# Kernel optimization log

Hardware: AMD Instinct MI355X
Metric: run time of the kernel (lower is better)

Reference implementation:

```python
import jax, jax.numpy as jnp
import numpy as np

QLEN, BSZ, D_MODEL = 1024, 4, 1024
N_HEAD, D_HEAD = 16, 64
RLEN = QLEN  # rlen == klen -> classic _rel_shift path
LN_EPS = 1e-5


def setup_inputs() -> dict:
    key = jax.random.key(0)
    ks = jax.random.split(key, 9)
    s = 0.02
    w = jax.random.normal(ks[0], (QLEN, BSZ, D_MODEL), jnp.float32)
    r = jax.random.normal(ks[1], (RLEN, D_MODEL), jnp.float32)
    # causal mask: True = masked (future positions)
    attn_mask = jnp.triu(jnp.ones((QLEN, QLEN), jnp.bool_), k=1)
    qkv_w = jax.random.normal(ks[2], (D_MODEL, 3 * N_HEAD * D_HEAD), jnp.float32) * s
    r_w = jax.random.normal(ks[3], (D_MODEL, N_HEAD * D_HEAD), jnp.float32) * s
    o_w = jax.random.normal(ks[4], (N_HEAD * D_HEAD, D_MODEL), jnp.float32) * s
    r_r_bias = jax.random.normal(ks[5], (N_HEAD, D_HEAD), jnp.float32) * s
    r_w_bias = jax.random.normal(ks[6], (N_HEAD, D_HEAD), jnp.float32) * s
    ln_g = jnp.ones((D_MODEL,), jnp.float32)
    ln_b = jnp.zeros((D_MODEL,), jnp.float32)
    return {"w": w, "r": r, "attn_mask": attn_mask, "qkv_w": qkv_w,
            "r_w": r_w, "o_w": o_w, "r_r_bias": r_r_bias,
            "r_w_bias": r_w_bias, "ln_g": ln_g, "ln_b": ln_b}


def _rel_shift(x):
    # x: [qlen, klen, bsz, n_head] -> Transformer-XL relative shift
    q, k, b, n = x.shape
    zero_pad = jnp.zeros((q, 1, b, n), x.dtype)
    x_padded = jnp.concatenate([zero_pad, x], axis=1)      # [q, k+1, b, n]
    x_padded = x_padded.reshape(k + 1, q, b, n)
    return x_padded[1:].reshape(q, k, b, n)


def _layer_norm(x, g, b):
    mu = jnp.mean(x, axis=-1, keepdims=True)
    var = jnp.mean(jnp.square(x - mu), axis=-1, keepdims=True)
    return (x - mu) * jax.lax.rsqrt(var + LN_EPS) * g + b


def reference(w, r, attn_mask, qkv_w, r_w, o_w, r_r_bias, r_w_bias, ln_g, ln_b):
    qlen, bsz, _ = w.shape
    H, D = r_r_bias.shape
    scale = 1.0 / D ** 0.5

    w_heads = w @ qkv_w                                    # [q, b, 3*H*D]
    q_h, k_h, v_h = jnp.split(w_heads, 3, axis=-1)
    q_h = q_h.reshape(qlen, bsz, H, D)
    k_h = k_h.reshape(qlen, bsz, H, D)
    v_h = v_h.reshape(qlen, bsz, H, D)
    r_k = (r @ r_w).reshape(-1, H, D)                      # [rlen, H, D]

    AC = jnp.einsum('ibnd,jbnd->ijbn', q_h + r_w_bias, k_h)
    BD = _rel_shift(jnp.einsum('ibnd,jnd->ijbn', q_h + r_r_bias, r_k))
    score = (AC + BD) * scale                              # [q, k, b, n]
    score = jnp.where(attn_mask[:, :, None, None], -1e30, score)

    prob = jax.nn.softmax(score, axis=1)
    vec = jnp.einsum('ijbn,jbnd->ibnd', prob, v_h).reshape(qlen, bsz, H * D)
    attn_out = vec @ o_w
    return _layer_norm(w + attn_out, ln_g, ln_b)
```

## Files before the change

kernel.cpp:

```cpp
#include <hip/hip_runtime.h>
#include <hip/hip_bf16.h>

#define SEQ    1024
#define BSZW   4
#define DMODEL 1024
#define NHEAD  16
#define DHEAD  64
#define MROWS  (SEQ*BSZW)
#define QKVN   (3*NHEAD*DHEAD)

typedef __attribute__((ext_vector_type(8))) short short8;
typedef __attribute__((ext_vector_type(4))) float f32x4;

__device__ __forceinline__ float bf2f(short s) {
    union { int i; float f; } u; u.i = ((int)(unsigned short)s) << 16; return u.f;
}
__device__ __forceinline__ short f2bf(float f) {
    union { float f; unsigned int u; } v; v.f = f;
    unsigned int r = v.u + 0x7FFFu + ((v.u >> 16) & 1u);
    return (short)(unsigned short)(r >> 16);
}

__device__ __forceinline__ void async16(const void* g, void* s) {
    __builtin_amdgcn_global_load_lds(
        (__attribute__((address_space(1))) void*)(g),
        (__attribute__((address_space(3))) void*)(s), 16, 0, 0);
}

__global__ __launch_bounds__(256) void conv_all(const float* __restrict__ w,
                                                const float* __restrict__ r,
                                                short* __restrict__ Wb,
                                                short* __restrict__ rb)
{
    int bx = blockIdx.x;
    const float* in; short* out; int idx;
    if (bx < 4096) { in = w; out = Wb; idx = (bx * 256 + threadIdx.x) * 4; }
    else           { in = r; out = rb; idx = ((bx - 4096) * 256 + threadIdx.x) * 4; }
    float4 v = *(const float4*)(in + idx);
    out[idx + 0] = f2bf(v.x);
    out[idx + 1] = f2bf(v.y);
    out[idx + 2] = f2bf(v.z);
    out[idx + 3] = f2bf(v.w);
}

__global__ __launch_bounds__(256) void trans_all(const float* __restrict__ qkv_w,
                                                 const float* __restrict__ r_w,
                                                 const float* __restrict__ o_w,
                                                 short* __restrict__ QKVt,
                                                 short* __restrict__ RWt,
                                                 short* __restrict__ OWt)
{
    const int z = blockIdx.z;
    const int bx = blockIdx.x, by = blockIdx.y;
    const float* in; short* out; int C;
    if (z == 0)      { in = qkv_w; out = QKVt; C = QKVN; }
    else if (z == 1) { in = r_w;   out = RWt;  C = DMODEL; if (bx >= 32) return; }
    else             { in = o_w;   out = OWt;  C = DMODEL; if (bx >= 32) return; }
    const int R = DMODEL;
    __shared__ short t[32][33];
    const int tid = threadIdx.x;
    const int r = tid >> 5, c = tid & 31;
    #pragma unroll
    for (int rr = 0; rr < 4; ++rr) {
        int rl = r + rr * 8;
        t[c][rl] = f2bf(in[(size_t)(by * 32 + rl) * C + bx * 32 + c]);
    }
    __syncthreads();
    #pragma unroll
    for (int rr = 0; rr < 4; ++rr) {
        int rl = r + rr * 8;
        out[(size_t)(bx * 32 + rl) * R + by * 32 + c] = t[rl][c];
    }
}

__global__ __launch_bounds__(256) void vtrans(const short* __restrict__ in,
                                              short* __restrict__ out)
{
    __shared__ short t[32][33];
    const int tid = threadIdx.x;
    const int r = tid >> 5, c = tid & 31;
    const int bx = blockIdx.x, by = blockIdx.y, bh = blockIdx.z;
    #pragma unroll
    for (int rr = 0; rr < 4; ++rr) {
        int rl = r + rr * 8;
        t[c][rl] = in[((size_t)bh * SEQ + bx * 32 + rl) * DHEAD + by * 32 + c];
    }
    __syncthreads();
    #pragma unroll
    for (int rr = 0; rr < 4; ++rr) {
        int rl = r + rr * 8;
        out[((size_t)bh * DHEAD + by * 32 + rl) * SEQ + bx * 32 + c] = t[rl][c];
    }
}

#define GEMM_LDS_CORE(A_, Bt_, K_)                                              \
    __shared__ short As[128 * 32];                                              \
    __shared__ short Bs[128 * 32];                                              \
    const int tid = threadIdx.x;                                                \
    const int w = tid >> 6, lane = tid & 63;                                    \
    const int L15 = lane & 15, quad = lane >> 4;                                \
    const int n0 = blockIdx.x * 128, m0 = blockIdx.y * 128;                     \
    const int mq = (w & 1) * 64, nq = (w >> 1) * 64;                            \
    f32x4 acc[4][4];                                                            \
    _Pragma("unroll")                                                           \
    for (int i = 0; i < 4; ++i)                                                 \
        _Pragma("unroll")                                                       \
        for (int j = 0; j < 4; ++j) acc[i][j] = (f32x4){0.f, 0.f, 0.f, 0.f};    \
    const int srow  = w * 16 + (lane >> 2);          \
    const int schnk = ((lane & 3) ^ (lane >> 4)) * 8;  \
    const int rpA = (quad ^ (L15 >> 2)) * 8;         \
    for (int k0 = 0; k0 < K_; k0 += 32) {                                       \
        __syncthreads();                                                        \
        _Pragma("unroll")                                                       \
        for (int q = 0; q < 2; ++q) {                                           \
            async16(A_ + (size_t)(m0 + q * 64 + srow) * K_ + k0 + schnk,        \
                    &As[(q * 64 + w * 16) * 32]);                               \
            async16(Bt_ + (size_t)(n0 + q * 64 + srow) * K_ + k0 + schnk,       \
                    &Bs[(q * 64 + w * 16) * 32]);                               \
        }                                                                       \
        __syncthreads();                                                        \
        short8 a[4], b[4];                                                      \
        _Pragma("unroll")                                                       \
        for (int rt = 0; rt < 4; ++rt)                                          \
            a[rt] = *(const short8*)&As[(mq + rt * 16 + L15) * 32 + rpA];       \
        _Pragma("unroll")                                                       \
        for (int ct = 0; ct < 4; ++ct)                                          \
            b[ct] = *(const short8*)&Bs[(nq + ct * 16 + L15) * 32 + rpA];       \
        _Pragma("unroll")                                                       \
        for (int rt = 0; rt < 4; ++rt)                                          \
            _Pragma("unroll")                                                   \
            for (int ct = 0; ct < 4; ++ct)                                      \
                acc[rt][ct] = __builtin_amdgcn_mfma_f32_16x16x32_bf16(          \
                    a[rt], b[ct], acc[rt][ct], 0, 0, 0);                        \
    }

__global__ __launch_bounds__(256) void qkv_mfma(const short* __restrict__ A,
                                                const short* __restrict__ Bt,
                                                const float* __restrict__ rwb,
                                                const float* __restrict__ rrb,
                                                short* __restrict__ Qwb,
                                                short* __restrict__ Qrb,
                                                short* __restrict__ Kb,
                                                short* __restrict__ Vb)
{
    GEMM_LDS_CORE(A, Bt, 1024)
    const int nb = n0 + nq;
    const int chunk = nb >> 10;
    const int h = (nb >> 6) & 15;
    float rw4[4], rr4[4];
    if (chunk == 0) {
        #pragma unroll
        for (int ct = 0; ct < 4; ++ct) {
            rw4[ct] = rwb[h * DHEAD + ct * 16 + L15];
            rr4[ct] = rrb[h * DHEAD + ct * 16 + L15];
        }
    }
    #pragma unroll
    for (int rt = 0; rt < 4; ++rt)
        #pragma unroll
        for (int g = 0; g < 4; ++g) {
            int m = m0 + mq + rt * 16 + quad * 4 + g;
            int qi = m >> 2, b = m & 3;
            size_t rowbase = ((size_t)(b * NHEAD + h) * SEQ + qi) * DHEAD;
            #pragma unroll
            for (int ct = 0; ct < 4; ++ct) {
                int d = ct * 16 + L15;
                float v = acc[rt][ct][g];
                if (chunk == 0) {
                    Qwb[rowbase + d] = f2bf(v + rw4[ct]);
                    Qrb[rowbase + d] = f2bf(v + rr4[ct]);
                } else if (chunk == 1) {
                    Kb[rowbase + d] = f2bf(v);
                } else {
                    Vb[rowbase + d] = f2bf(v);
                }
            }
        }
}

__global__ __launch_bounds__(256) void rk_mfma(const short* __restrict__ A,
                                               const short* __restrict__ Bt,
                                               short* __restrict__ RK)
{
    GEMM_LDS_CORE(A, Bt, 1024)
    const int h = (n0 + nq) >> 6;
    #pragma unroll
    for (int rt = 0; rt < 4; ++rt)
        #pragma unroll
        for (int g = 0; g < 4; ++g) {
            int m = m0 + mq + rt * 16 + quad * 4 + g;
            #pragma unroll
            for (int ct = 0; ct < 4; ++ct) {
                int d = ct * 16 + L15;
                RK[((size_t)h * SEQ + m) * DHEAD + d] = f2bf(acc[rt][ct][g]);
            }
        }
}

__global__ __launch_bounds__(256) void oproj_mfma(const short* __restrict__ A,
                                                  const short* __restrict__ Bt,
                                                  float* __restrict__ C)
{
    GEMM_LDS_CORE(A, Bt, 1024)
    #pragma unroll
    for (int rt = 0; rt < 4; ++rt)
        #pragma unroll
        for (int g = 0; g < 4; ++g) {
            int m = m0 + mq + rt * 16 + quad * 4 + g;
            #pragma unroll
            for (int ct = 0; ct < 4; ++ct)
                C[(size_t)m * DMODEL + n0 + nq + ct * 16 + L15] = acc[rt][ct][g];
        }
}

__global__ __launch_bounds__(256) void attn_mfma(const short* __restrict__ Qw,
                                                 const short* __restrict__ Qr,
                                                 const short* __restrict__ Kg,
                                                 const short* __restrict__ Vt,
                                                 const short* __restrict__ RK,
                                                 short* __restrict__ ATT)
{
    __shared__ short Ks[2][64 * 64];
    __shared__ short Vts[2][64 * 64];
    __shared__ short Pbuf[4][16][136];

    const int tid  = threadIdx.x;
    const int w    = tid >> 6;
    const int lane = tid & 63;
    const int L15  = lane & 15;
    const int quad = lane >> 4;
    const int bh   = blockIdx.x;
    const int itA  = blockIdx.y;
    const int itB  = 15 - itA;
    const int h    = bh & (NHEAD - 1);
    const int b    = bh >> 4;
    const int C    = 63 - 16 * w;

    const short* Kbh = Kg + (size_t)bh * SEQ * DHEAD;
    const short* Vbh = Vt + (size_t)bh * DHEAD * SEQ;
    const short* Rh  = RK + (size_t)h * SEQ * DHEAD;

    const int srow  = w * 8 + (lane >> 3);
    const int schnk = ((lane & 7) ^ (lane >> 3)) * 8;
    const int rp0 = ((quad)     ^ (L15 & 7)) * 8;
    const int rp1 = ((quad + 4) ^ (L15 & 7)) * 8;

    int it = itA;
    short8 qwf[2], qrf[2];
    {
        const short* qb = Qw + ((size_t)bh * SEQ + it * 64 + w * 16 + L15) * DHEAD + quad * 8;
        qwf[0] = *(const short8*)qb;
        qwf[1] = *(const short8*)(qb + 32);
        const short* qc = Qr + ((size_t)bh * SEQ + it * 64 + w * 16 + L15) * DHEAD + quad * 8;
        qrf[0] = *(const short8*)qc;
        qrf[1] = *(const short8*)(qc + 32);
    }

    f32x4 O[4];
    float mrow[4], lrow[4];
    #pragma unroll
    for (int c = 0; c < 4; ++c) { O[c] = (f32x4){0.f, 0.f, 0.f, 0.f}; }
    #pragma unroll
    for (int g = 0; g < 4; ++g) { mrow[g] = -1e30f; lrow[g] = 0.f; }

    #pragma unroll
    for (int q = 0; q < 2; ++q) {
        int rr = q * 32 + srow;
        async16(Kbh + (size_t)rr * DHEAD + schnk,   &Ks[0][(q * 32 + w * 8) * 64]);
        async16(Vbh + (size_t)rr * SEQ + schnk,     &Vts[0][(q * 32 + w * 8) * 64]);
    }

    for (int k = 0; k < 17; ++k) {
        if (k == itA + 1) {
            #pragma unroll
            for (int g = 0; g < 4; ++g) {
                float inv = 1.0f / lrow[g];
                int i = itA * 64 + w * 16 + quad * 4 + g;
                #pragma unroll
                for (int ct = 0; ct < 4; ++ct)
                    ATT[((size_t)i * BSZW + b) * DMODEL + h * DHEAD + ct * 16 + L15] =
                        f2bf(O[ct][g] * inv);
            }
            it = itB;
            #pragma unroll
            for (int c = 0; c < 4; ++c) O[c] = (f32x4){0.f, 0.f, 0.f, 0.f};
            #pragma unroll
            for (int g = 0; g < 4; ++g) { mrow[g] = -1e30f; lrow[g] = 0.f; }
            const short* qb = Qw + ((size_t)bh * SEQ + it * 64 + w * 16 + L15) * DHEAD + quad * 8;
            qwf[0] = *(const short8*)qb;
            qwf[1] = *(const short8*)(qb + 32);
            const short* qc = Qr + ((size_t)bh * SEQ + it * 64 + w * 16 + L15) * DHEAD + quad * 8;
            qrf[0] = *(const short8*)qc;
            qrf[1] = *(const short8*)(qc + 32);
        }
        const int jt  = (k <= itA) ? k : (k - itA - 1);
        const int buf = k & 1;
        const int j0  = jt * 64;
        const int rel0 = 960 + 64 * (jt - it);

        __syncthreads();

        if (k < 16) {
            const int kn  = k + 1;
            const int jtn = (kn <= itA) ? kn : (kn - itA - 1);
            const int j0n = jtn * 64;
            #pragma unroll
            for (int q = 0; q < 2; ++q) {
                int rr = q * 32 + srow;
                async16(Kbh + (size_t)(j0n + rr) * DHEAD + schnk,
                        &Ks[buf ^ 1][(q * 32 + w * 8) * 64]);
                async16(Vbh + (size_t)rr * SEQ + j0n + schnk,
                        &Vts[buf ^ 1][(q * 32 + w * 8) * 64]);
            }
        }

        short8 rb0[5], rb1[5];
        #pragma unroll
        for (int cp = 0; cp < 5; ++cp) {
            int ct  = (3 - w) + cp;
            int rel = rel0 + ct * 16 + L15;
            rel = (rel > SEQ - 1) ? (SEQ - 1) : rel;
            const short* rp = Rh + (size_t)rel * DHEAD + quad * 8;
            rb0[cp] = *(const short8*)rp;
            rb1[cp] = *(const short8*)(rp + 32);
        }

        f32x4 S[4];
        #pragma unroll
        for (int ct = 0; ct < 4; ++ct) {
            short8 b0 = *(const short8*)&Ks[buf][(ct * 16 + L15) * 64 + rp0];
            short8 b1 = *(const short8*)&Ks[buf][(ct * 16 + L15) * 64 + rp1];
            f32x4 acc = (f32x4){0.f, 0.f, 0.f, 0.f};
            acc = __builtin_amdgcn_mfma_f32_16x16x32_bf16(qwf[0], b0, acc, 0, 0, 0);
            acc = __builtin_amdgcn_mfma_f32_16x16x32_bf16(qwf[1], b1, acc, 0, 0, 0);
            S[ct] = acc;
        }

        #pragma unroll
        for (int cp = 0; cp < 5; ++cp) {
            int ct = (3 - w) + cp;
            f32x4 p = (f32x4){0.f, 0.f, 0.f, 0.f};
            p = __builtin_amdgcn_mfma_f32_16x16x32_bf16(qrf[0], rb0[cp], p, 0, 0, 0);
            p = __builtin_amdgcn_mfma_f32_16x16x32_bf16(qrf[1], rb1[cp], p, 0, 0, 0);
            #pragma unroll
            for (int g = 0; g < 4; ++g)
                Pbuf[w][quad * 4 + g][ct * 16 + L15] = f2bf(p[g]);
        }

        #pragma unroll
        for (int ct = 0; ct < 4; ++ct) {
            #pragma unroll
            for (int g = 0; g < 4; ++g) {
                int r = quad * 4 + g;
                int t = ct * 16 + L15 - r + C;
                float bd = bf2f(Pbuf[w][r][t]);
                S[ct][g] = (S[ct][g] + bd) * 0.125f;
            }
        }
        if (jt == it) {
            #pragma unroll
            for (int ct = 0; ct < 4; ++ct)
                #pragma unroll
                for (int g = 0; g < 4; ++g) {
                    int i = it * 64 + w * 16 + quad * 4 + g;
                    int j = j0 + ct * 16 + L15;
                    if (j > i) S[ct][g] = -1e30f;
                }
        }

        float mt[4];
        #pragma unroll
        for (int g = 0; g < 4; ++g)
            mt[g] = fmaxf(fmaxf(S[0][g], S[1][g]), fmaxf(S[2][g], S[3][g]));
        #pragma unroll
        for (int off = 1; off < 16; off <<= 1)
            #pragma unroll
            for (int g = 0; g < 4; ++g)
                mt[g] = fmaxf(mt[g], __shfl_xor(mt[g], off, 64));

        float al[4];
        #pragma unroll
        for (int g = 0; g < 4; ++g) {
            float mn = fmaxf(mrow[g], mt[g]);
            al[g] = __expf(mrow[g] - mn);
            mrow[g] = mn;
        }
        #pragma unroll
        for (int ct = 0; ct < 4; ++ct)
            #pragma unroll
            for (int g = 0; g < 4; ++g)
                S[ct][g] = __expf(S[ct][g] - mrow[g]);

        float rs[4];
        #pragma unroll
        for (int g = 0; g < 4; ++g)
            rs[g] = (S[0][g] + S[1][g]) + (S[2][g] + S[3][g]);
        #pragma unroll
        for (int off = 1; off < 16; off <<= 1)
            #pragma unroll
            for (int g = 0; g < 4; ++g)
                rs[g] += __shfl_xor(rs[g], off, 64);
        #pragma unroll
        for (int g = 0; g < 4; ++g)
            lrow[g] = lrow[g] * al[g] + rs[g];
        #pragma unroll
        for (int ct = 0; ct < 4; ++ct)
            #pragma unroll
            for (int g = 0; g < 4; ++g)
                O[ct][g] *= al[g];

        #pragma unroll
        for (int ct = 0; ct < 4; ++ct)
            #pragma unroll
            for (int g = 0; g < 4; ++g)
                Pbuf[w][quad * 4 + g][ct * 16 + L15] = f2bf(S[ct][g]);
        short8 pa0 = *(const short8*)&Pbuf[w][L15][quad * 8];
        short8 pa1 = *(const short8*)&Pbuf[w][L15][32 + quad * 8];

        #pragma unroll
        for (int ct = 0; ct < 4; ++ct) {
            short8 v0 = *(const short8*)&Vts[buf][(ct * 16 + L15) * 64 + rp0];
            short8 v1 = *(const short8*)&Vts[buf][(ct * 16 + L15) * 64 + rp1];
            O[ct] = __builtin_amdgcn_mfma_f32_16x16x32_bf16(pa0, v0, O[ct], 0, 0, 0);
            O[ct] = __builtin_amdgcn_mfma_f32_16x16x32_bf16(pa1, v1, O[ct], 0, 0, 0);
        }
    }

    #pragma unroll
    for (int g = 0; g < 4; ++g) {
        float inv = 1.0f / lrow[g];
        int i = itB * 64 + w * 16 + quad * 4 + g;
        #pragma unroll
        for (int ct = 0; ct < 4; ++ct)
            ATT[((size_t)i * BSZW + b) * DMODEL + h * DHEAD + ct * 16 + L15] =
                f2bf(O[ct][g] * inv);
    }
}

__global__ __launch_bounds__(256) void ln_kernel(const float* __restrict__ w,
                                                 const float* __restrict__ AO,
                                                 const float* __restrict__ g,
                                                 const float* __restrict__ bb,
                                                 float* __restrict__ out)
{
    __shared__ float red[256];
    __shared__ float sh_mu, sh_rs;
    const int m = blockIdx.x;
    const int tid = threadIdx.x;
    float x[4];
    #pragma unroll
    for (int k = 0; k < 4; ++k) {
        int j = tid + 256 * k;
        x[k] = w[(size_t)m * DMODEL + j] + AO[(size_t)m * DMODEL + j];
    }
    red[tid] = x[0] + x[1] + x[2] + x[3];
    __syncthreads();
    for (int st = 128; st > 0; st >>= 1) {
        if (tid < st) red[tid] += red[tid + st];
        __syncthreads();
    }
    if (tid == 0) sh_mu = red[0] * (1.0f / DMODEL);
    __syncthreads();
    const float mu = sh_mu;
    float v = 0.0f;
    #pragma unroll
    for (int k = 0; k < 4; ++k) { float d = x[k] - mu; v += d * d; }
    red[tid] = v;
    __syncthreads();
    for (int st = 128; st > 0; st >>= 1) {
        if (tid < st) red[tid] += red[tid + st];
        __syncthreads();
    }
    if (tid == 0) sh_rs = rsqrtf(red[0] * (1.0f / DMODEL) + 1e-5f);
    __syncthreads();
    const float rs = sh_rs;
    #pragma unroll
    for (int k = 0; k < 4; ++k) {
        int j = tid + 256 * k;
        out[(size_t)m * DMODEL + j] = (x[k] - mu) * rs * g[j] + bb[j];
    }
}

extern "C" void kernel_launch(void* const* d_in, const int* in_sizes, int n_in,
                              void* d_out, int out_size, void* d_ws, size_t ws_size,
                              hipStream_t stream)
{
    (void)in_sizes; (void)n_in; (void)out_size; (void)ws_size;
    const float* w     = (const float*)d_in[0];
    const float* r     = (const float*)d_in[1];
    const float* qkv_w = (const float*)d_in[3];
    const float* r_w   = (const float*)d_in[4];
    const float* o_w   = (const float*)d_in[5];
    const float* rrb   = (const float*)d_in[6];
    const float* rwb   = (const float*)d_in[7];
    const float* ln_g  = (const float*)d_in[8];
    const float* ln_b  = (const float*)d_in[9];
    float* out = (float*)d_out;

    const size_t M1 = 1024 * 1024;
    short* Wb   = (short*)d_ws;
    short* QKVt = Wb   + 4 * M1;
    short* rb   = QKVt + 3 * M1;
    short* RWt  = rb   + 1 * M1;
    short* OWt  = RWt  + 1 * M1;
    short* Qwb  = OWt  + 1 * M1;
    short* Qrb  = Qwb  + 4 * M1;
    short* Kb   = Qrb  + 4 * M1;
    short* Vb   = Kb   + 4 * M1;
    short* Vtb  = Vb   + 4 * M1;
    short* RKb  = Vtb  + 4 * M1;
    short* ATTb = Vb;
    float* AO   = (float*)d_ws;

    conv_all<<<5120, 256, 0, stream>>>(w, r, Wb, rb);
    trans_all<<<dim3(QKVN / 32, DMODEL / 32, 3), 256, 0, stream>>>(qkv_w, r_w, o_w,
                                                                   QKVt, RWt, OWt);

    qkv_mfma<<<dim3(QKVN / 128, MROWS / 128), 256, 0, stream>>>(Wb, QKVt, rwb, rrb,
                                                                Qwb, Qrb, Kb, Vb);
    vtrans<<<dim3(SEQ / 32, DHEAD / 32, BSZW * NHEAD), 256, 0, stream>>>(Vb, Vtb);
    rk_mfma<<<dim3(DMODEL / 128, SEQ / 128), 256, 0, stream>>>(rb, RWt, RKb);
    attn_mfma<<<dim3(BSZW * NHEAD, 8), 256, 0, stream>>>(Qwb, Qrb, Kb, Vtb, RKb, ATTb);
    oproj_mfma<<<dim3(DMODEL / 128, MROWS / 128), 256, 0, stream>>>(ATTb, OWt, AO);
    ln_kernel<<<MROWS, 256, 0, stream>>>(w, AO, ln_g, ln_b, out);
}
```

Before: 262.5 us.

## Merge QKV and R-K GEMMs, narrow o-proj tiles, shuffle rel-shift, vectorize LN

The QKV and positional-key GEMMs now share one launch, with extra grid rows for R-K and surplus blocks exiting early. The output projection uses 128x64 tiles so the grid has twice as many blocks and fills more CUs. In attention, the relative-shift of the BD scores now uses ds_bpermute lane shuffles in registers instead of a bf16 round-trip through LDS, which also drops that rounding. The layer-norm kernel switches to float4 loads and stores. These are several unrelated changes aimed at launch count, occupancy and LDS traffic.

```diff
diff --git a/kernel.cpp b/kernel.cpp
--- a/kernel.cpp
+++ b/kernel.cpp
@@ -93,22 +93,20 @@
     }
 }
 
-#define GEMM_LDS_CORE(A_, Bt_, K_)                                              \
+#define GEMM_BODY_128(A_, Bt_, K_)                                             \
     __shared__ short As[128 * 32];                                              \
     __shared__ short Bs[128 * 32];                                              \
-    const int tid = threadIdx.x;                                                \
     const int w = tid >> 6, lane = tid & 63;                                    \
     const int L15 = lane & 15, quad = lane >> 4;                                \
-    const int n0 = blockIdx.x * 128, m0 = blockIdx.y * 128;                     \
     const int mq = (w & 1) * 64, nq = (w >> 1) * 64;                            \
     f32x4 acc[4][4];                                                            \
     _Pragma("unroll")                                                           \
     for (int i = 0; i < 4; ++i)                                                 \
         _Pragma("unroll")                                                       \
         for (int j = 0; j < 4; ++j) acc[i][j] = (f32x4){0.f, 0.f, 0.f, 0.f};    \
-    const int srow  = w * 16 + (lane >> 2);          \
-    const int schnk = ((lane & 3) ^ (lane >> 4)) * 8;  \
-    const int rpA = (quad ^ (L15 >> 2)) * 8;         \
+    const int srow  = w * 16 + (lane >> 2);                                     \
+    const int schnk = ((lane & 3) ^ (lane >> 4)) * 8;                           \
+    const int rpA = (quad ^ (L15 >> 2)) * 8;                                    \
     for (int k0 = 0; k0 < K_; k0 += 32) {                                       \
         __syncthreads();                                                        \
         _Pragma("unroll")                                                       \
@@ -134,16 +132,42 @@
                     a[rt], b[ct], acc[rt][ct], 0, 0, 0);                        \
     }
 
-__global__ __launch_bounds__(256) void qkv_mfma(const short* __restrict__ A,
-                                                const short* __restrict__ Bt,
-                                                const float* __restrict__ rwb,
-                                                const float* __restrict__ rrb,
-                                                short* __restrict__ Qwb,
-                                                short* __restrict__ Qrb,
-                                                short* __restrict__ Kb,
-                                                short* __restrict__ Vb)
-{
-    GEMM_LDS_CORE(A, Bt, 1024)
+__global__ __launch_bounds__(256) void qkv_rk_mfma(const short* __restrict__ Wb,
+                                                   const short* __restrict__ QKVt,
+                                                   const short* __restrict__ rbuf,
+                                                   const short* __restrict__ RWt,
+                                                   const float* __restrict__ rwb,
+                                                   const float* __restrict__ rrb,
+                                                   short* __restrict__ Qwb,
+                                                   short* __restrict__ Qrb,
+                                                   short* __restrict__ Kb,
+                                                   short* __restrict__ Vb,
+                                                   short* __restrict__ RK)
+{
+    const int tid = threadIdx.x;
+    const int by = blockIdx.y;
+    const bool isrk = (by >= 32);
+    if (isrk && blockIdx.x >= 8) return;
+    const short* A_  = isrk ? rbuf : Wb;
+    const short* Bt_ = isrk ? RWt : QKVt;
+    const int m0 = (isrk ? (by - 32) : by) * 128;
+    const int n0 = blockIdx.x * 128;
+    GEMM_BODY_128(A_, Bt_, 1024)
+
+    if (isrk) {
+        const int h = (n0 + nq) >> 6;
+        #pragma unroll
+        for (int rt = 0; rt < 4; ++rt)
+            #pragma unroll
+            for (int g = 0; g < 4; ++g) {
+                int m = m0 + mq + rt * 16 + quad * 4 + g;
+                #pragma unroll
+                for (int ct = 0; ct < 4; ++ct)
+                    RK[((size_t)h * SEQ + m) * DHEAD + ct * 16 + L15] =
+                        f2bf(acc[rt][ct][g]);
+            }
+        return;
+    }
     const int nb = n0 + nq;
     const int chunk = nb >> 10;
     const int h = (nb >> 6) & 15;
@@ -178,38 +202,55 @@
         }
 }
 
-__global__ __launch_bounds__(256) void rk_mfma(const short* __restrict__ A,
-                                               const short* __restrict__ Bt,
-                                               short* __restrict__ RK)
-{
-    GEMM_LDS_CORE(A, Bt, 1024)
-    const int h = (n0 + nq) >> 6;
-    #pragma unroll
-    for (int rt = 0; rt < 4; ++rt)
-        #pragma unroll
-        for (int g = 0; g < 4; ++g) {
-            int m = m0 + mq + rt * 16 + quad * 4 + g;
-            #pragma unroll
-            for (int ct = 0; ct < 4; ++ct) {
-                int d = ct * 16 + L15;
-                RK[((size_t)h * SEQ + m) * DHEAD + d] = f2bf(acc[rt][ct][g]);
-            }
-        }
-}
-
 __global__ __launch_bounds__(256) void oproj_mfma(const short* __restrict__ A,
                                                   const short* __restrict__ Bt,
                                                   float* __restrict__ C)
 {
-    GEMM_LDS_CORE(A, Bt, 1024)
-    #pragma unroll
-    for (int rt = 0; rt < 4; ++rt)
+    __shared__ short As[128 * 32];
+    __shared__ short Bs[64 * 32];
+    const int tid = threadIdx.x;
+    const int w = tid >> 6, lane = tid & 63;
+    const int L15 = lane & 15, quad = lane >> 4;
+    const int n0 = blockIdx.x * 64, m0 = blockIdx.y * 128;
+    const int mq = w * 32;
+    f32x4 acc[2][4];
+    #pragma unroll
+    for (int i = 0; i < 2; ++i)
+        #pragma unroll
+        for (int j = 0; j < 4; ++j) acc[i][j] = (f32x4){0.f, 0.f, 0.f, 0.f};
+    const int srow  = w * 16 + (lane >> 2);
+    const int schnk = ((lane & 3) ^ (lane >> 4)) * 8;
+    const int rpA = (quad ^ (L15 >> 2)) * 8;
+    for (int k0 = 0; k0 < 1024; k0 += 32) {
+        __syncthreads();
+        #pragma unroll
+        for (int q = 0; q < 2; ++q)
+            async16(A + (size_t)(m0 + q * 64 + srow) * 1024 + k0 + schnk,
+                    &As[(q * 64 + w * 16) * 32]);
+        async16(Bt + (size_t)(n0 + srow) * 1024 + k0 + schnk, &Bs[(w * 16) * 32]);
+        __syncthreads();
+        short8 a[2], b[4];
+        #pragma unroll
+        for (int rt = 0; rt < 2; ++rt)
+            a[rt] = *(const short8*)&As[(mq + rt * 16 + L15) * 32 + rpA];
+        #pragma unroll
+        for (int ct = 0; ct < 4; ++ct)
+            b[ct] = *(const short8*)&Bs[(ct * 16 + L15) * 32 + rpA];
+        #pragma unroll
+        for (int rt = 0; rt < 2; ++rt)
+            #pragma unroll
+            for (int ct = 0; ct < 4; ++ct)
+                acc[rt][ct] = __builtin_amdgcn_mfma_f32_16x16x32_bf16(
+                    a[rt], b[ct], acc[rt][ct], 0, 0, 0);
+    }
+    #pragma unroll
+    for (int rt = 0; rt < 2; ++rt)
         #pragma unroll
         for (int g = 0; g < 4; ++g) {
             int m = m0 + mq + rt * 16 + quad * 4 + g;
             #pragma unroll
             for (int ct = 0; ct < 4; ++ct)
-                C[(size_t)m * DMODEL + n0 + nq + ct * 16 + L15] = acc[rt][ct][g];
+                C[(size_t)m * DMODEL + n0 + ct * 16 + L15] = acc[rt][ct][g];
         }
 }
 
@@ -222,7 +263,7 @@
 {
     __shared__ short Ks[2][64 * 64];
     __shared__ short Vts[2][64 * 64];
-    __shared__ short Pbuf[4][16][136];
+    __shared__ short Pv[4][16][72];
 
     const int tid  = threadIdx.x;
     const int w    = tid >> 6;
@@ -245,6 +286,14 @@
     const int rp0 = ((quad)     ^ (L15 & 7)) * 8;
     const int rp1 = ((quad + 4) ^ (L15 & 7)) * 8;
 
+    int ib[4]; bool selhi[4];
+    #pragma unroll
+    for (int g = 0; g < 4; ++g) {
+        int r = quad * 4 + g;
+        ib[g] = (((quad << 4) | ((L15 + 15 - r) & 15)) << 2);
+        selhi[g] = (L15 > r);
+    }
+
     int it = itA;
     short8 qwf[2], qrf[2];
     {
@@ -266,8 +315,8 @@
     #pragma unroll
     for (int q = 0; q < 2; ++q) {
         int rr = q * 32 + srow;
-        async16(Kbh + (size_t)rr * DHEAD + schnk,   &Ks[0][(q * 32 + w * 8) * 64]);
-        async16(Vbh + (size_t)rr * SEQ + schnk,     &Vts[0][(q * 32 + w * 8) * 64]);
+        async16(Kbh + (size_t)rr * DHEAD + schnk, &Ks[0][(q * 32 + w * 8) * 64]);
+        async16(Vbh + (size_t)rr * SEQ + schnk,   &Vts[0][(q * 32 + w * 8) * 64]);
     }
 
     for (int k = 0; k < 17; ++k) {
@@ -336,27 +385,30 @@
             S[ct] = acc;
         }
 
+        f32x4 p[5];
         #pragma unroll
         for (int cp = 0; cp < 5; ++cp) {
-            int ct = (3 - w) + cp;
-            f32x4 p = (f32x4){0.f, 0.f, 0.f, 0.f};
-            p = __builtin_amdgcn_mfma_f32_16x16x32_bf16(qrf[0], rb0[cp], p, 0, 0, 0);
-            p = __builtin_amdgcn_mfma_f32_16x16x32_bf16(qrf[1], rb1[cp], p, 0, 0, 0);
+            f32x4 pp = (f32x4){0.f, 0.f, 0.f, 0.f};
+            pp = __builtin_amdgcn_mfma_f32_16x16x32_bf16(qrf[0], rb0[cp], pp, 0, 0, 0);
+            pp = __builtin_amdgcn_mfma_f32_16x16x32_bf16(qrf[1], rb1[cp], pp, 0, 0, 0);
+            p[cp] = pp;
+        }
+
+        float qq[5][4];
+        #pragma unroll
+        for (int cp = 0; cp < 5; ++cp)
             #pragma unroll
             for (int g = 0; g < 4; ++g)
-                Pbuf[w][quad * 4 + g][ct * 16 + L15] = f2bf(p[g]);
-        }
-
-        #pragma unroll
-        for (int ct = 0; ct < 4; ++ct) {
+                qq[cp][g] = __int_as_float(
+                    __builtin_amdgcn_ds_bpermute(ib[g], __float_as_int(p[cp][g])));
+        #pragma unroll
+        for (int ct = 0; ct < 4; ++ct)
             #pragma unroll
             for (int g = 0; g < 4; ++g) {
-                int r = quad * 4 + g;
-                int t = ct * 16 + L15 - r + C;
-                float bd = bf2f(Pbuf[w][r][t]);
+                float bd = selhi[g] ? qq[ct + 1][g] : qq[ct][g];
                 S[ct][g] = (S[ct][g] + bd) * 0.125f;
             }
-        }
+
         if (jt == it) {
             #pragma unroll
             for (int ct = 0; ct < 4; ++ct)
@@ -413,9 +465,9 @@
         for (int ct = 0; ct < 4; ++ct)
             #pragma unroll
             for (int g = 0; g < 4; ++g)
-                Pbuf[w][quad * 4 + g][ct * 16 + L15] = f2bf(S[ct][g]);
-        short8 pa0 = *(const short8*)&Pbuf[w][L15][quad * 8];
-        short8 pa1 = *(const short8*)&Pbuf[w][L15][32 + quad * 8];
+                Pv[w][quad * 4 + g][ct * 16 + L15] = f2bf(S[ct][g]);
+        short8 pa0 = *(const short8*)&Pv[w][L15][quad * 8];
+        short8 pa1 = *(const short8*)&Pv[w][L15][32 + quad * 8];
 
         #pragma unroll
         for (int ct = 0; ct < 4; ++ct) {
@@ -447,12 +499,10 @@
     __shared__ float sh_mu, sh_rs;
     const int m = blockIdx.x;
     const int tid = threadIdx.x;
-    float x[4];
-    #pragma unroll
-    for (int k = 0; k < 4; ++k) {
-        int j = tid + 256 * k;
-        x[k] = w[(size_t)m * DMODEL + j] + AO[(size_t)m * DMODEL + j];
-    }
+    const int j0 = tid * 4;
+    float4 xw = *(const float4*)(w + (size_t)m * DMODEL + j0);
+    float4 xa = *(const float4*)(AO + (size_t)m * DMODEL + j0);
+    float x[4] = {xw.x + xa.x, xw.y + xa.y, xw.z + xa.z, xw.w + xa.w};
     red[tid] = x[0] + x[1] + x[2] + x[3];
     __syncthreads();
     for (int st = 128; st > 0; st >>= 1) {
@@ -474,11 +524,14 @@
     if (tid == 0) sh_rs = rsqrtf(red[0] * (1.0f / DMODEL) + 1e-5f);
     __syncthreads();
     const float rs = sh_rs;
-    #pragma unroll
-    for (int k = 0; k < 4; ++k) {
-        int j = tid + 256 * k;
-        out[(size_t)m * DMODEL + j] = (x[k] - mu) * rs * g[j] + bb[j];
-    }
+    float4 g4 = *(const float4*)(g + j0);
+    float4 b4 = *(const float4*)(bb + j0);
+    float4 o4;
+    o4.x = (x[0] - mu) * rs * g4.x + b4.x;
+    o4.y = (x[1] - mu) * rs * g4.y + b4.y;
+    o4.z = (x[2] - mu) * rs * g4.z + b4.z;
+    o4.w = (x[3] - mu) * rs * g4.w + b4.w;
+    *(float4*)(out + (size_t)m * DMODEL + j0) = o4;
 }
 
 extern "C" void kernel_launch(void* const* d_in, const int* in_sizes, int n_in,
@@ -516,11 +569,11 @@
     trans_all<<<dim3(QKVN / 32, DMODEL / 32, 3), 256, 0, stream>>>(qkv_w, r_w, o_w,
                                                                    QKVt, RWt, OWt);
 
-    qkv_mfma<<<dim3(QKVN / 128, MROWS / 128), 256, 0, stream>>>(Wb, QKVt, rwb, rrb,
-                                                                Qwb, Qrb, Kb, Vb);
+    qkv_rk_mfma<<<dim3(QKVN / 128, 40), 256, 0, stream>>>(Wb, QKVt, rb, RWt,
+                                                          rwb, rrb,
+                                                          Qwb, Qrb, Kb, Vb, RKb);
     vtrans<<<dim3(SEQ / 32, DHEAD / 32, BSZW * NHEAD), 256, 0, stream>>>(Vb, Vtb);
-    rk_mfma<<<dim3(DMODEL / 128, SEQ / 128), 256, 0, stream>>>(rb, RWt, RKb);
     attn_mfma<<<dim3(BSZW * NHEAD, 8), 256, 0, stream>>>(Qwb, Qrb, Kb, Vtb, RKb, ATTb);
-    oproj_mfma<<<dim3(DMODEL / 128, MROWS / 128), 256, 0, stream>>>(ATTb, OWt, AO);
+    oproj_mfma<<<dim3(DMODEL / 64, MROWS / 128), 256, 0, stream>>>(ATTb, OWt, AO);
     ln_kernel<<<MROWS, 256, 0, stream>>>(w, AO, ln_g, ln_b, out);
 }
```

Result: no change. 261.8 us (-0.3%).
